# Optimization experiments

Measured on AMD Instinct MI355X. Metric: run time of the kernel, lower is better.

Reference implementation:

```python
import jax, jax.numpy as jnp
import numpy as np

N_NODES = 50000
N_EDGES = 1600000
IN_DIM = 128
HID = 128
SHARED = 64
N_GRAPHS = 2048


def setup_inputs() -> dict:
    key = jax.random.key(0)
    ks = jax.random.split(key, 16)
    x = jax.random.normal(ks[0], (N_NODES, IN_DIM), dtype=jnp.float32)
    edge_index = jax.random.randint(ks[1], (2, N_EDGES), 0, N_NODES, dtype=jnp.int64)
    batch = jnp.sort(jax.random.randint(ks[2], (N_NODES,), 0, N_GRAPHS, dtype=jnp.int64))

    def lin(k, fan_in, fan_out):
        bound = 1.0 / np.sqrt(fan_in)
        kw, kb = jax.random.split(k)
        W = jax.random.uniform(kw, (fan_in, fan_out), minval=-bound, maxval=bound, dtype=jnp.float32)
        b = jax.random.uniform(kb, (fan_out,), minval=-bound, maxval=bound, dtype=jnp.float32)
        return W, b

    W1a, b1a = lin(ks[3], IN_DIM, HID)
    W1b, b1b = lin(ks[4], HID, HID)
    W2a, b2a = lin(ks[5], HID, HID)
    W2b, b2b = lin(ks[6], HID, HID)
    Ws, bs = lin(ks[7], HID, SHARED)
    WlS, blS = lin(ks[8], SHARED, 1)
    WlP, blP = lin(ks[9], SHARED, 1)
    WnR, bnR = lin(ks[10], SHARED, 1)
    return dict(x=x, edge_index=edge_index, batch=batch,
                W1a=W1a, b1a=b1a, W1b=W1b, b1b=b1b,
                W2a=W2a, b2a=b2a, W2b=W2b, b2b=b2b,
                Ws=Ws, bs=bs, WlS=WlS, blS=blS, WlP=WlP, blP=blP, WnR=WnR, bnR=bnR)


def gin_conv(x, src, dst, Wa, ba, Wb, bb):
    # GINConv (eps=0): h_i = MLP(x_i + sum_{j->i} x_j)
    agg = jax.ops.segment_sum(x[src], dst, num_segments=N_NODES)
    h = x + agg
    h = jax.nn.relu(h @ Wa + ba)
    return h @ Wb + bb


def reference(x, edge_index, batch, W1a, b1a, W1b, b1b, W2a, b2a, W2b, b2b,
              Ws, bs, WlS, blS, WlP, blP, WnR, bnR):
    src, dst = edge_index[0], edge_index[1]
    h = jax.nn.relu(gin_conv(x, src, dst, W1a, b1a, W1b, b1b))
    h = jax.nn.relu(gin_conv(h, src, dst, W2a, b2a, W2b, b2b))
    # global mean pool over graph ids
    sums = jax.ops.segment_sum(h, batch, num_segments=N_GRAPHS)
    counts = jax.ops.segment_sum(jnp.ones((h.shape[0],), h.dtype), batch, num_segments=N_GRAPHS)
    pooled = sums / jnp.maximum(counts, 1.0)[:, None]
    g = jax.nn.relu(pooled @ Ws + bs)
    out_logS = (g @ WlS + blS)[:, 0]
    out_logP = (g @ WlP + blP)[:, 0]
    out_NR = (g @ WnR + bnR)[:, 0]
    return (out_logS, out_logP, out_NR)
```

## Files before the change

### kernel.cpp

```cpp
#include <hip/hip_runtime.h>
#include <hip/hip_bf16.h>


#define IN_DIM 128
#define NFINE 256
#define BIN_EPB 4096
#define SRCCH 16
#define NSLOT 3200
#define SPT 7

typedef float  f32x4  __attribute__((ext_vector_type(4)));
typedef short  bf16x4 __attribute__((ext_vector_type(4)));
typedef short  bf16x8 __attribute__((ext_vector_type(8)));

__device__ __forceinline__ unsigned short bf16_rne(float v) {
    unsigned u = __float_as_uint(v);
    unsigned t = u + 0x7fffu + ((u >> 16) & 1u);
    return (unsigned short)(t >> 16);
}


__global__ __launch_bounds__(256) void f32_to_bf16_kernel(
    const float4* __restrict__ in, uint4* __restrict__ out, int n8)
{
    int i = blockIdx.x * 256 + threadIdx.x;
    if (i >= n8) return;
    float4 a = in[i * 2];
    float4 b = in[i * 2 + 1];
    float v[8] = {a.x, a.y, a.z, a.w, b.x, b.y, b.z, b.w};
    unsigned r[4];
#pragma unroll
    for (int j = 0; j < 4; ++j)
        r[j] = (unsigned)bf16_rne(v[j * 2]) | ((unsigned)bf16_rne(v[j * 2 + 1]) << 16);
    out[i] = make_uint4(r[0], r[1], r[2], r[3]);
}


__global__ __launch_bounds__(256) void conv_weights_kernel(
    const float* __restrict__ W0, const float* __restrict__ W1,
    const float* __restrict__ W2, const float* __restrict__ W3,
    unsigned short* __restrict__ Wh, unsigned short* __restrict__ Wl)
{
    int m   = blockIdx.x >> 6;
    int idx = (blockIdx.x & 63) * 256 + threadIdx.x;
    const float* W = (m == 0) ? W0 : (m == 1) ? W1 : (m == 2) ? W2 : W3;
    int k = idx >> 7, n = idx & 127;
    float v = W[idx];
    unsigned short hh = bf16_rne(v);
    float hf = __uint_as_float(((unsigned)hh) << 16);
    unsigned short ll = bf16_rne(v - hf);
    Wh[m * 16384 + n * 128 + k] = hh;
    Wl[m * 16384 + n * 128 + k] = ll;
}


__device__ __forceinline__ int bucket_lo(int b, int n_nodes) {
    return (int)(((long long)b * n_nodes + NFINE - 1) / NFINE);
}

__global__ __launch_bounds__(256) void bin_kernel(
    const int* __restrict__ src, const int* __restrict__ dst,
    int* __restrict__ buckets, int* __restrict__ bcur,
    int n_edges, int n_nodes, int cap)
{
    __shared__ int cnt[NFINE];
    __shared__ int base[NFINE];
    cnt[threadIdx.x] = 0;
    __syncthreads();

    const int e0 = blockIdx.x * BIN_EPB + threadIdx.x * 16;
    int ne = n_edges - e0;
    if (ne < 0) ne = 0;
    if (ne > 16) ne = 16;

    int d[16], s[16], off[16];
    if (ne == 16) {
#pragma unroll
        for (int q = 0; q < 4; ++q) {
            int4 dv = *(const int4*)(dst + e0 + q * 4);
            int4 sv = *(const int4*)(src + e0 + q * 4);
            d[q * 4 + 0] = dv.x; d[q * 4 + 1] = dv.y;
            d[q * 4 + 2] = dv.z; d[q * 4 + 3] = dv.w;
            s[q * 4 + 0] = sv.x; s[q * 4 + 1] = sv.y;
            s[q * 4 + 2] = sv.z; s[q * 4 + 3] = sv.w;
        }
    } else {
#pragma unroll
        for (int j = 0; j < 16; ++j) {
            d[j] = (j < ne) ? dst[e0 + j] : 0;
            s[j] = (j < ne) ? src[e0 + j] : 0;
        }
    }
#pragma unroll
    for (int j = 0; j < 16; ++j)
        if (j < ne) {
            int b = (int)(((long long)d[j] * NFINE) / n_nodes);
            off[j] = atomicAdd(&cnt[b], 1);
        }
    __syncthreads();
    base[threadIdx.x] = atomicAdd(&bcur[threadIdx.x], cnt[threadIdx.x]);
    __syncthreads();
#pragma unroll
    for (int j = 0; j < 16; ++j)
        if (j < ne) {
            int b = (int)(((long long)d[j] * NFINE) / n_nodes);
            int pack = ((d[j] - bucket_lo(b, n_nodes)) << 16) | s[j];
            buckets[(size_t)b * cap + base[b] + off[j]] = pack;
        }
}

__global__ __launch_bounds__(512) void csr_fused_kernel(
    const int* __restrict__ buckets, const int* __restrict__ bcnt,
    int* __restrict__ row_start, int* __restrict__ csr_src,
    int cap, int n_nodes, int n_edges)
{
    __shared__ int bc[NFINE];
    __shared__ int h[NSLOT];
    __shared__ int tsum[512];
    __shared__ int bbase_s;

    const int b = blockIdx.x;
    const int t = threadIdx.x;
    const int lo_n = bucket_lo(b, n_nodes);
    const int hi_n = bucket_lo(b + 1, n_nodes);
    const int sl = hi_n - lo_n;

    if (t < NFINE) bc[t] = bcnt[t];
    for (int i = t; i < NSLOT; i += 512) h[i] = 0;
    __syncthreads();
    if (t == 0) {
        int s = 0;
        for (int i = 0; i < b; ++i) s += bc[i];
        bbase_s = s;
    }
    const int nb = bc[b];
    const int* bp = buckets + (size_t)b * cap;
    __syncthreads();

    for (int i = t; i < nb; i += 512) {
        int v = bp[i];
        int key = (v >> 16) * SRCCH + (int)(((long long)(v & 0xFFFF) * SRCCH) / n_nodes);
        atomicAdd(&h[key], 1);
    }
    __syncthreads();

    int base = 0;
#pragma unroll
    for (int j = 0; j < SPT; ++j) {
        int slot = t * SPT + j;
        if (slot < NSLOT) {
            int v = h[slot];
            h[slot] = base;
            base += v;
        }
    }
    tsum[t] = base;
    __syncthreads();
    for (int off = 1; off < 512; off <<= 1) {
        int tmp = (t >= off) ? tsum[t - off] : 0;
        __syncthreads();
        tsum[t] += tmp;
        __syncthreads();
    }
    int texcl = tsum[t] - base + bbase_s;
#pragma unroll
    for (int j = 0; j < SPT; ++j) {
        int slot = t * SPT + j;
        if (slot < NSLOT) h[slot] += texcl;
    }
    __syncthreads();
    for (int i = t; i < sl; i += 512) row_start[lo_n + i] = h[i * SRCCH];
    if (b == NFINE - 1 && t == 0) row_start[n_nodes] = n_edges;
    __syncthreads();

    for (int i = t; i < nb; i += 512) {
        int v = bp[i];
        int key = (v >> 16) * SRCCH + (int)(((long long)(v & 0xFFFF) * SRCCH) / n_nodes);
        csr_src[atomicAdd(&h[key], 1)] = v & 0xFFFF;
    }
}


__device__ __forceinline__ void add_row8(float acc[8], uint4 r) {
    union { unsigned u; float f; } c;
    c.u = r.x << 16;         acc[0] += c.f;
    c.u = r.x & 0xffff0000u; acc[1] += c.f;
    c.u = r.y << 16;         acc[2] += c.f;
    c.u = r.y & 0xffff0000u; acc[3] += c.f;
    c.u = r.z << 16;         acc[4] += c.f;
    c.u = r.z & 0xffff0000u; acc[5] += c.f;
    c.u = r.w << 16;         acc[6] += c.f;
    c.u = r.w & 0xffff0000u; acc[7] += c.f;
}

__global__ __launch_bounds__(256) void gather_agg_bf16_kernel(
    const float* __restrict__ xf,
    const uint4* __restrict__ xb,
    const int* __restrict__ row_start, const int* __restrict__ csr_src,
    float* __restrict__ out, int n_nodes)
{
    int t = blockIdx.x * 256 + threadIdx.x;
    int node = t >> 4;
    int lane = t & 15;
    if (node >= n_nodes) return;
    int lo = row_start[node];
    int hi = row_start[node + 1];

    const f32x4* xfr = (const f32x4*)(xf + (size_t)node * IN_DIM + lane * 8);
    f32x4 a0 = __builtin_nontemporal_load(xfr);
    f32x4 a1 = __builtin_nontemporal_load(xfr + 1);
    float acc[8] = {a0.x, a0.y, a0.z, a0.w, a1.x, a1.y, a1.z, a1.w};

    int e = lo;
    for (; e + 3 < hi; e += 4) {
        int s0 = csr_src[e];
        int s1 = csr_src[e + 1];
        int s2 = csr_src[e + 2];
        int s3 = csr_src[e + 3];
        uint4 r0 = xb[(size_t)s0 * 16 + lane];
        uint4 r1 = xb[(size_t)s1 * 16 + lane];
        uint4 r2 = xb[(size_t)s2 * 16 + lane];
        uint4 r3 = xb[(size_t)s3 * 16 + lane];
        add_row8(acc, r0);
        add_row8(acc, r1);
        add_row8(acc, r2);
        add_row8(acc, r3);
    }
    for (; e < hi; ++e) {
        uint4 r = xb[(size_t)csr_src[e] * 16 + lane];
        add_row8(acc, r);
    }

    f32x4 o0 = {acc[0], acc[1], acc[2], acc[3]};
    f32x4 o1 = {acc[4], acc[5], acc[6], acc[7]};
    f32x4* op = (f32x4*)(out + (size_t)node * IN_DIM + lane * 8);
    __builtin_nontemporal_store(o0, op);
    __builtin_nontemporal_store(o1, op + 1);
}

#define HSTRIDE 132

template <bool EMIT_BF16>
__global__ __launch_bounds__(256) void fused_mlp_kernel(
    const float* __restrict__ A,
    const unsigned short* __restrict__ Wa_h, const unsigned short* __restrict__ Wa_l,
    const float* __restrict__ ba,
    const unsigned short* __restrict__ Wb_h, const unsigned short* __restrict__ Wb_l,
    const float* __restrict__ bb,
    float* __restrict__ C, unsigned short* __restrict__ Cb, int M)
{
    __shared__ __align__(16) unsigned short Hh[64][HSTRIDE];
    __shared__ __align__(16) unsigned short Hl[64][HSTRIDE];

    const int t    = threadIdx.x;
    const int wave = t >> 6;
    const int lane = t & 63;
    const int l15  = lane & 15;
    const int quad = lane >> 4;
    const int rw   = (wave & 1) * 32;
    const int cw   = (wave >> 1) * 64;
    const int row0 = blockIdx.x * 64 + rw;

    bf16x8 ah[2][4], al[2][4];

#pragma unroll
    for (int ti = 0; ti < 2; ++ti) {
        int ar = row0 + ti * 16 + l15;
        const float* ap = A + (size_t)((ar < M) ? ar : (M - 1)) * IN_DIM + quad * 8;
        f32x4 av[8];
#pragma unroll
        for (int k0c = 0; k0c < 4; ++k0c) {
            av[k0c * 2]     = *(const f32x4*)(ap + k0c * 32);
            av[k0c * 2 + 1] = *(const f32x4*)(ap + k0c * 32 + 4);
        }
#pragma unroll
        for (int k0c = 0; k0c < 4; ++k0c) {
            float v[8] = {av[k0c * 2].x, av[k0c * 2].y, av[k0c * 2].z, av[k0c * 2].w,
                          av[k0c * 2 + 1].x, av[k0c * 2 + 1].y,
                          av[k0c * 2 + 1].z, av[k0c * 2 + 1].w};
            unsigned short hh[8], ll[8];
#pragma unroll
            for (int j = 0; j < 8; ++j) {
                unsigned short h = bf16_rne(v[j]);
                hh[j] = h;
                ll[j] = bf16_rne(v[j] - __uint_as_float(((unsigned)h) << 16));
            }
            ah[ti][k0c] = *(const bf16x8*)hh;
            al[ti][k0c] = *(const bf16x8*)ll;
        }
    }

    f32x4 acc[2][4];
#pragma unroll
    for (int ti = 0; ti < 2; ++ti)
#pragma unroll
        for (int ct = 0; ct < 4; ++ct) acc[ti][ct] = {0.f, 0.f, 0.f, 0.f};

#pragma unroll
    for (int ct = 0; ct < 4; ++ct) {
        const unsigned short* wph = Wa_h + (size_t)(cw + ct * 16 + l15) * IN_DIM + quad * 8;
        const unsigned short* wpl = Wa_l + (size_t)(cw + ct * 16 + l15) * IN_DIM + quad * 8;
        bf16x8 wh[4], wl[4];
#pragma unroll
        for (int k0c = 0; k0c < 4; ++k0c) {
            wh[k0c] = *(const bf16x8*)(wph + k0c * 32);
            wl[k0c] = *(const bf16x8*)(wpl + k0c * 32);
        }
#pragma unroll
        for (int k0c = 0; k0c < 4; ++k0c) {
            acc[0][ct] = __builtin_amdgcn_mfma_f32_16x16x32_bf16(ah[0][k0c], wh[k0c], acc[0][ct], 0, 0, 0);
            acc[1][ct] = __builtin_amdgcn_mfma_f32_16x16x32_bf16(ah[1][k0c], wh[k0c], acc[1][ct], 0, 0, 0);
            acc[0][ct] = __builtin_amdgcn_mfma_f32_16x16x32_bf16(al[0][k0c], wh[k0c], acc[0][ct], 0, 0, 0);
            acc[1][ct] = __builtin_amdgcn_mfma_f32_16x16x32_bf16(al[1][k0c], wh[k0c], acc[1][ct], 0, 0, 0);
            acc[0][ct] = __builtin_amdgcn_mfma_f32_16x16x32_bf16(ah[0][k0c], wl[k0c], acc[0][ct], 0, 0, 0);
            acc[1][ct] = __builtin_amdgcn_mfma_f32_16x16x32_bf16(ah[1][k0c], wl[k0c], acc[1][ct], 0, 0, 0);
        }
    }

#pragma unroll
    for (int ti = 0; ti < 2; ++ti) {
#pragma unroll
        for (int ct = 0; ct < 4; ++ct) {
            int col = cw + ct * 16 + l15;
            float b = ba[col];
#pragma unroll
            for (int r = 0; r < 4; ++r) {
                int rl = rw + ti * 16 + quad * 4 + r;
                float v = fmaxf(acc[ti][ct][r] + b, 0.f);
                unsigned short hh = bf16_rne(v);
                Hh[rl][col] = hh;
                Hl[rl][col] = bf16_rne(v - __uint_as_float(((unsigned)hh) << 16));
            }
            acc[ti][ct] = {0.f, 0.f, 0.f, 0.f};
        }
    }
    __syncthreads();

#pragma unroll
    for (int ti = 0; ti < 2; ++ti) {
        const int hr = rw + ti * 16 + l15;
#pragma unroll
        for (int k0c = 0; k0c < 4; ++k0c) {
            const int hk = k0c * 32 + quad * 8;
            bf16x4 h0 = *(const bf16x4*)&Hh[hr][hk];
            bf16x4 h1 = *(const bf16x4*)&Hh[hr][hk + 4];
            bf16x4 l0 = *(const bf16x4*)&Hl[hr][hk];
            bf16x4 l1 = *(const bf16x4*)&Hl[hr][hk + 4];
            ah[ti][k0c] = __builtin_shufflevector(h0, h1, 0, 1, 2, 3, 4, 5, 6, 7);
            al[ti][k0c] = __builtin_shufflevector(l0, l1, 0, 1, 2, 3, 4, 5, 6, 7);
        }
    }

#pragma unroll
    for (int ct = 0; ct < 4; ++ct) {
        const unsigned short* wph = Wb_h + (size_t)(cw + ct * 16 + l15) * IN_DIM + quad * 8;
        const unsigned short* wpl = Wb_l + (size_t)(cw + ct * 16 + l15) * IN_DIM + quad * 8;
        bf16x8 wh[4], wl[4];
#pragma unroll
        for (int k0c = 0; k0c < 4; ++k0c) {
            wh[k0c] = *(const bf16x8*)(wph + k0c * 32);
            wl[k0c] = *(const bf16x8*)(wpl + k0c * 32);
        }
#pragma unroll
        for (int k0c = 0; k0c < 4; ++k0c) {
            acc[0][ct] = __builtin_amdgcn_mfma_f32_16x16x32_bf16(ah[0][k0c], wh[k0c], acc[0][ct], 0, 0, 0);
            acc[1][ct] = __builtin_amdgcn_mfma_f32_16x16x32_bf16(ah[1][k0c], wh[k0c], acc[1][ct], 0, 0, 0);
            acc[0][ct] = __builtin_amdgcn_mfma_f32_16x16x32_bf16(al[0][k0c], wh[k0c], acc[0][ct], 0, 0, 0);
            acc[1][ct] = __builtin_amdgcn_mfma_f32_16x16x32_bf16(al[1][k0c], wh[k0c], acc[1][ct], 0, 0, 0);
            acc[0][ct] = __builtin_amdgcn_mfma_f32_16x16x32_bf16(ah[0][k0c], wl[k0c], acc[0][ct], 0, 0, 0);
            acc[1][ct] = __builtin_amdgcn_mfma_f32_16x16x32_bf16(ah[1][k0c], wl[k0c], acc[1][ct], 0, 0, 0);
        }
    }

#pragma unroll
    for (int ti = 0; ti < 2; ++ti) {
        const int rbase = row0 + ti * 16 + quad * 4;
#pragma unroll
        for (int ct = 0; ct < 4; ++ct) {
            int col = cw + ct * 16 + l15;
            float b = bb[col];
#pragma unroll
            for (int r = 0; r < 4; ++r) {
                int row = rbase + r;
                if (row < M) {
                    float o = fmaxf(acc[ti][ct][r] + b, 0.f);
                    C[(size_t)row * IN_DIM + col] = o;
                    if (EMIT_BF16)
                        Cb[(size_t)row * IN_DIM + col] = bf16_rne(o);
                }
            }
        }
    }
}


__device__ __forceinline__ int lower_bound_i(const int* __restrict__ a, int n, int v) {
    int lo = 0, hi = n;
    while (lo < hi) {
        int mid = (lo + hi) >> 1;
        if (a[mid] < v) lo = mid + 1; else hi = mid;
    }
    return lo;
}

__global__ __launch_bounds__(128) void pool_kernel(
    const float* __restrict__ h, const int* __restrict__ batch,
    float* __restrict__ pooled, int n_nodes, int n_graphs)
{
    int g = blockIdx.x;
    int lo = lower_bound_i(batch, n_nodes, g);
    int hi = lower_bound_i(batch, n_nodes, g + 1);
    int j = threadIdx.x;
    float acc = 0.f;
    for (int i = lo; i < hi; ++i)
        acc += h[(size_t)i * IN_DIM + j];
    float cnt = (float)(hi - lo);
    pooled[(size_t)g * IN_DIM + j] = acc / fmaxf(cnt, 1.0f);
}

__global__ __launch_bounds__(64) void head_kernel(
    const float* __restrict__ pooled,
    const float* __restrict__ Ws,  const float* __restrict__ bs,
    const float* __restrict__ WlS, const float* __restrict__ blS,
    const float* __restrict__ WlP, const float* __restrict__ blP,
    const float* __restrict__ WnR, const float* __restrict__ bnR,
    float* __restrict__ out, int n_graphs)
{
    int g = blockIdx.x;
    int j = threadIdx.x;
    const float* p = pooled + (size_t)g * IN_DIM;
    float acc = bs[j];
#pragma unroll 8
    for (int k = 0; k < IN_DIM; ++k)
        acc = fmaf(p[k], Ws[k * 64 + j], acc);
    float gj = fmaxf(acc, 0.f);
    float s1 = gj * WlS[j];
    float s2 = gj * WlP[j];
    float s3 = gj * WnR[j];
#pragma unroll
    for (int off = 32; off > 0; off >>= 1) {
        s1 += __shfl_down(s1, off);
        s2 += __shfl_down(s2, off);
        s3 += __shfl_down(s3, off);
    }
    if (j == 0) {
        out[g]                = s1 + blS[0];
        out[n_graphs + g]     = s2 + blP[0];
        out[2 * n_graphs + g] = s3 + bnR[0];
    }
}


extern "C" void kernel_launch(void* const* d_in, const int* in_sizes, int n_in,
                              void* d_out, int out_size, void* d_ws, size_t ws_size,
                              hipStream_t stream)
{
    const float* x   = (const float*)d_in[0];
    const int*   ei  = (const int*)d_in[1];
    const int*   bat = (const int*)d_in[2];
    const float* W1a = (const float*)d_in[3];
    const float* b1a = (const float*)d_in[4];
    const float* W1b = (const float*)d_in[5];
    const float* b1b = (const float*)d_in[6];
    const float* W2a = (const float*)d_in[7];
    const float* b2a = (const float*)d_in[8];
    const float* W2b = (const float*)d_in[9];
    const float* b2b = (const float*)d_in[10];
    const float* Ws  = (const float*)d_in[11];
    const float* bs  = (const float*)d_in[12];
    const float* WlS = (const float*)d_in[13];
    const float* blS = (const float*)d_in[14];
    const float* WlP = (const float*)d_in[15];
    const float* blP = (const float*)d_in[16];
    const float* WnR = (const float*)d_in[17];
    const float* bnR = (const float*)d_in[18];

    const int n_nodes  = in_sizes[0] / IN_DIM;
    const int n_edges  = in_sizes[1] / 2;
    const int n_graphs = out_size / 3;
    const int* src = ei;
    const int* dst = ei + n_edges;

    const size_t node_elems   = (size_t)n_nodes * IN_DIM;
    const size_t pooled_elems = (size_t)n_graphs * IN_DIM;

    float* xbf    = (float*)d_ws;
    float* buf2   = xbf  + node_elems;
    float* bufA   = buf2 + node_elems;
    float* pooled = bufA + node_elems;
    int* row_start = (int*)(pooled + pooled_elems);
    int* bcur      = row_start + (n_nodes + 1);
    int* csr_src   = bcur + NFINE;
    unsigned short* wt_h = (unsigned short*)(csr_src + n_edges);
    unsigned short* wt_l = wt_h + 4 * 16384;

    unsigned short* xb = (unsigned short*)xbf;
    const int cap = n_edges / NFINE + 1024;
    int* buckets = (int*)bufA;

    const int gatherblocks = (int)(((size_t)n_nodes * 16 + 255) / 256);
    const int mlpblocks = (n_nodes + 63) / 64;
    const int binblocks = (n_edges + BIN_EPB - 1) / BIN_EPB;
    const int n8 = (int)(node_elems / 8);
    const int cvtblocks = (n8 + 255) / 256;

    conv_weights_kernel<<<256, 256, 0, stream>>>(W1a, W1b, W2a, W2b, wt_h, wt_l);
    hipMemsetAsync(bcur, 0, NFINE * sizeof(int), stream);
    bin_kernel<<<binblocks, 256, 0, stream>>>(src, dst, buckets, bcur,
                                              n_edges, n_nodes, cap);
    csr_fused_kernel<<<NFINE, 512, 0, stream>>>(buckets, bcur, row_start,
                                                csr_src, cap, n_nodes, n_edges);

    f32_to_bf16_kernel<<<cvtblocks, 256, 0, stream>>>((const float4*)x, (uint4*)xb, n8);
    gather_agg_bf16_kernel<<<gatherblocks, 256, 0, stream>>>(
        x, (const uint4*)xb, row_start, csr_src, bufA, n_nodes);
    fused_mlp_kernel<true><<<mlpblocks, 256, 0, stream>>>(
        bufA, wt_h, wt_l, b1a, wt_h + 16384, wt_l + 16384, b1b,
        buf2, xb, n_nodes);

    gather_agg_bf16_kernel<<<gatherblocks, 256, 0, stream>>>(
        buf2, (const uint4*)xb, row_start, csr_src, bufA, n_nodes);
    fused_mlp_kernel<false><<<mlpblocks, 256, 0, stream>>>(
        bufA, wt_h + 2 * 16384, wt_l + 2 * 16384, b2a,
        wt_h + 3 * 16384, wt_l + 3 * 16384, b2b,
        buf2, nullptr, n_nodes);

    pool_kernel<<<n_graphs, 128, 0, stream>>>(buf2, bat, pooled, n_nodes, n_graphs);
    head_kernel<<<n_graphs, 64, 0, stream>>>(pooled, Ws, bs, WlS, blS, WlP, blP,
                                             WnR, bnR, (float*)d_out, n_graphs);
}
```

Measured before the change: 375.8 us.

## Fuse neighbor gather-aggregation into GIN MLP kernel via shared-memory staging

Merges the separate gather-aggregate kernel into the fused MLP kernel. Each 64-row block first sums its rows' self features and bf16 neighbor rows, then writes the hi/lo bf16 split into LDS, where the MFMA stages read it. This removes the fp32 aggregate round-trip through global memory and two launches per layer. The second layer reads from a separate bf16 copy so it can overwrite buf2 in place. The cost is fewer independent gather threads in flight per CU, because LDS use grows and each block walks its 64 nodes in four serial passes, so the random-access gather may hide latency less well.

Result: slower. 419.6 us (+11.6%).

```diff
diff --git a/kernel.cpp b/kernel.cpp
--- a/kernel.cpp
+++ b/kernel.cpp
@@ -8,9 +8,9 @@
 #define SRCCH 16
 #define NSLOT 3200
 #define SPT 7
+#define HSTRIDE 136
 
 typedef float  f32x4  __attribute__((ext_vector_type(4)));
-typedef short  bf16x4 __attribute__((ext_vector_type(4)));
 typedef short  bf16x8 __attribute__((ext_vector_type(8)));
 
 __device__ __forceinline__ unsigned short bf16_rne(float v) {
@@ -193,66 +193,67 @@
     c.u = r.w & 0xffff0000u; acc[7] += c.f;
 }
 
-__global__ __launch_bounds__(256) void gather_agg_bf16_kernel(
-    const float* __restrict__ xf,
+template <bool EMIT_BF16>
+__global__ __launch_bounds__(256) void fused_gin_layer_kernel(
+    const float* __restrict__ Aself,
     const uint4* __restrict__ xb,
     const int* __restrict__ row_start, const int* __restrict__ csr_src,
-    float* __restrict__ out, int n_nodes)
-{
-    int t = blockIdx.x * 256 + threadIdx.x;
-    int node = t >> 4;
-    int lane = t & 15;
-    if (node >= n_nodes) return;
-    int lo = row_start[node];
-    int hi = row_start[node + 1];
-
-    const f32x4* xfr = (const f32x4*)(xf + (size_t)node * IN_DIM + lane * 8);
-    f32x4 a0 = __builtin_nontemporal_load(xfr);
-    f32x4 a1 = __builtin_nontemporal_load(xfr + 1);
-    float acc[8] = {a0.x, a0.y, a0.z, a0.w, a1.x, a1.y, a1.z, a1.w};
-
-    int e = lo;
-    for (; e + 3 < hi; e += 4) {
-        int s0 = csr_src[e];
-        int s1 = csr_src[e + 1];
-        int s2 = csr_src[e + 2];
-        int s3 = csr_src[e + 3];
-        uint4 r0 = xb[(size_t)s0 * 16 + lane];
-        uint4 r1 = xb[(size_t)s1 * 16 + lane];
-        uint4 r2 = xb[(size_t)s2 * 16 + lane];
-        uint4 r3 = xb[(size_t)s3 * 16 + lane];
-        add_row8(acc, r0);
-        add_row8(acc, r1);
-        add_row8(acc, r2);
-        add_row8(acc, r3);
-    }
-    for (; e < hi; ++e) {
-        uint4 r = xb[(size_t)csr_src[e] * 16 + lane];
-        add_row8(acc, r);
-    }
-
-    f32x4 o0 = {acc[0], acc[1], acc[2], acc[3]};
-    f32x4 o1 = {acc[4], acc[5], acc[6], acc[7]};
-    f32x4* op = (f32x4*)(out + (size_t)node * IN_DIM + lane * 8);
-    __builtin_nontemporal_store(o0, op);
-    __builtin_nontemporal_store(o1, op + 1);
-}
-
-#define HSTRIDE 132
-
-template <bool EMIT_BF16>
-__global__ __launch_bounds__(256) void fused_mlp_kernel(
-    const float* __restrict__ A,
     const unsigned short* __restrict__ Wa_h, const unsigned short* __restrict__ Wa_l,
     const float* __restrict__ ba,
     const unsigned short* __restrict__ Wb_h, const unsigned short* __restrict__ Wb_l,
     const float* __restrict__ bb,
     float* __restrict__ C, unsigned short* __restrict__ Cb, int M)
 {
-    __shared__ __align__(16) unsigned short Hh[64][HSTRIDE];
-    __shared__ __align__(16) unsigned short Hl[64][HSTRIDE];
-
-    const int t    = threadIdx.x;
+    __shared__ __align__(16) unsigned short Ah[64][HSTRIDE];
+    __shared__ __align__(16) unsigned short Al[64][HSTRIDE];
+
+    const int t = threadIdx.x;
+
+    {
+        const int gl = t & 15;
+        const int gn = t >> 4;
+        for (int rl = gn; rl < 64; rl += 16) {
+            const int node = blockIdx.x * 64 + rl;
+            float acc[8] = {0.f, 0.f, 0.f, 0.f, 0.f, 0.f, 0.f, 0.f};
+            if (node < M) {
+                const f32x4* sp = (const f32x4*)(Aself + (size_t)node * IN_DIM + gl * 8);
+                f32x4 a0 = sp[0];
+                f32x4 a1 = sp[1];
+                acc[0] = a0.x; acc[1] = a0.y; acc[2] = a0.z; acc[3] = a0.w;
+                acc[4] = a1.x; acc[5] = a1.y; acc[6] = a1.z; acc[7] = a1.w;
+                int lo = row_start[node];
+                int hi = row_start[node + 1];
+                int e = lo;
+                for (; e + 3 < hi; e += 4) {
+                    int s0 = csr_src[e];
+                    int s1 = csr_src[e + 1];
+                    int s2 = csr_src[e + 2];
+                    int s3 = csr_src[e + 3];
+                    uint4 r0 = xb[(size_t)s0 * 16 + gl];
+                    uint4 r1 = xb[(size_t)s1 * 16 + gl];
+                    uint4 r2 = xb[(size_t)s2 * 16 + gl];
+                    uint4 r3 = xb[(size_t)s3 * 16 + gl];
+                    add_row8(acc, r0);
+                    add_row8(acc, r1);
+                    add_row8(acc, r2);
+                    add_row8(acc, r3);
+                }
+                for (; e < hi; ++e)
+                    add_row8(acc, xb[(size_t)csr_src[e] * 16 + gl]);
+            }
+            unsigned short hh[8], ll[8];
+#pragma unroll
+            for (int j = 0; j < 8; ++j) {
+                unsigned short h = bf16_rne(acc[j]);
+                hh[j] = h;
+                ll[j] = bf16_rne(acc[j] - __uint_as_float(((unsigned)h) << 16));
+            }
+            *(uint4*)&Ah[rl][gl * 8] = *(uint4*)hh;
+            *(uint4*)&Al[rl][gl * 8] = *(uint4*)ll;
+        }
+    }
+    __syncthreads();
+
     const int wave = t >> 6;
     const int lane = t & 63;
     const int l15  = lane & 15;
@@ -262,33 +263,17 @@
     const int row0 = blockIdx.x * 64 + rw;
 
     bf16x8 ah[2][4], al[2][4];
-
 #pragma unroll
     for (int ti = 0; ti < 2; ++ti) {
-        int ar = row0 + ti * 16 + l15;
-        const float* ap = A + (size_t)((ar < M) ? ar : (M - 1)) * IN_DIM + quad * 8;
-        f32x4 av[8];
+        const int hr = rw + ti * 16 + l15;
 #pragma unroll
         for (int k0c = 0; k0c < 4; ++k0c) {
-            av[k0c * 2]     = *(const f32x4*)(ap + k0c * 32);
-            av[k0c * 2 + 1] = *(const f32x4*)(ap + k0c * 32 + 4);
-        }
-#pragma unroll
-        for (int k0c = 0; k0c < 4; ++k0c) {
-            float v[8] = {av[k0c * 2].x, av[k0c * 2].y, av[k0c * 2].z, av[k0c * 2].w,
-                          av[k0c * 2 + 1].x, av[k0c * 2 + 1].y,
-                          av[k0c * 2 + 1].z, av[k0c * 2 + 1].w};
-            unsigned short hh[8], ll[8];
-#pragma unroll
-            for (int j = 0; j < 8; ++j) {
-                unsigned short h = bf16_rne(v[j]);
-                hh[j] = h;
-                ll[j] = bf16_rne(v[j] - __uint_as_float(((unsigned)h) << 16));
-            }
-            ah[ti][k0c] = *(const bf16x8*)hh;
-            al[ti][k0c] = *(const bf16x8*)ll;
-        }
-    }
+            const int hk = k0c * 32 + quad * 8;
+            ah[ti][k0c] = *(const bf16x8*)&Ah[hr][hk];
+            al[ti][k0c] = *(const bf16x8*)&Al[hr][hk];
+        }
+    }
+    __syncthreads();
 
     f32x4 acc[2][4];
 #pragma unroll
@@ -328,8 +313,8 @@
                 int rl = rw + ti * 16 + quad * 4 + r;
                 float v = fmaxf(acc[ti][ct][r] + b, 0.f);
                 unsigned short hh = bf16_rne(v);
-                Hh[rl][col] = hh;
-                Hl[rl][col] = bf16_rne(v - __uint_as_float(((unsigned)hh) << 16));
+                Ah[rl][col] = hh;
+                Al[rl][col] = bf16_rne(v - __uint_as_float(((unsigned)hh) << 16));
             }
             acc[ti][ct] = {0.f, 0.f, 0.f, 0.f};
         }
@@ -342,12 +327,8 @@
 #pragma unroll
         for (int k0c = 0; k0c < 4; ++k0c) {
             const int hk = k0c * 32 + quad * 8;
-            bf16x4 h0 = *(const bf16x4*)&Hh[hr][hk];
-            bf16x4 h1 = *(const bf16x4*)&Hh[hr][hk + 4];
-            bf16x4 l0 = *(const bf16x4*)&Hl[hr][hk];
-            bf16x4 l1 = *(const bf16x4*)&Hl[hr][hk + 4];
-            ah[ti][k0c] = __builtin_shufflevector(h0, h1, 0, 1, 2, 3, 4, 5, 6, 7);
-            al[ti][k0c] = __builtin_shufflevector(l0, l1, 0, 1, 2, 3, 4, 5, 6, 7);
+            ah[ti][k0c] = *(const bf16x8*)&Ah[hr][hk];
+            al[ti][k0c] = *(const bf16x8*)&Al[hr][hk];
         }
     }
 
@@ -494,12 +475,12 @@
     unsigned short* wt_h = (unsigned short*)(csr_src + n_edges);
     unsigned short* wt_l = wt_h + 4 * 16384;
 
-    unsigned short* xb = (unsigned short*)xbf;
+    unsigned short* xb  = (unsigned short*)xbf;
+    unsigned short* xb2 = xb + node_elems;
     const int cap = n_edges / NFINE + 1024;
     int* buckets = (int*)bufA;
 
-    const int gatherblocks = (int)(((size_t)n_nodes * 16 + 255) / 256);
-    const int mlpblocks = (n_nodes + 63) / 64;
+    const int layerblocks = (n_nodes + 63) / 64;
     const int binblocks = (n_edges + BIN_EPB - 1) / BIN_EPB;
     const int n8 = (int)(node_elems / 8);
     const int cvtblocks = (n8 + 255) / 256;
@@ -512,16 +493,14 @@
                                                 csr_src, cap, n_nodes, n_edges);
 
     f32_to_bf16_kernel<<<cvtblocks, 256, 0, stream>>>((const float4*)x, (uint4*)xb, n8);
-    gather_agg_bf16_kernel<<<gatherblocks, 256, 0, stream>>>(
-        x, (const uint4*)xb, row_start, csr_src, bufA, n_nodes);
-    fused_mlp_kernel<true><<<mlpblocks, 256, 0, stream>>>(
-        bufA, wt_h, wt_l, b1a, wt_h + 16384, wt_l + 16384, b1b,
-        buf2, xb, n_nodes);
-
-    gather_agg_bf16_kernel<<<gatherblocks, 256, 0, stream>>>(
-        buf2, (const uint4*)xb, row_start, csr_src, bufA, n_nodes);
-    fused_mlp_kernel<false><<<mlpblocks, 256, 0, stream>>>(
-        bufA, wt_h + 2 * 16384, wt_l + 2 * 16384, b2a,
+    fused_gin_layer_kernel<true><<<layerblocks, 256, 0, stream>>>(
+        x, (const uint4*)xb, row_start, csr_src,
+        wt_h, wt_l, b1a, wt_h + 16384, wt_l + 16384, b1b,
+        buf2, xb2, n_nodes);
+
+    fused_gin_layer_kernel<false><<<layerblocks, 256, 0, stream>>>(
+        buf2, (const uint4*)xb2, row_start, csr_src,
+        wt_h + 2 * 16384, wt_l + 2 * 16384, b2a,
         wt_h + 3 * 16384, wt_l + 3 * 16384, b2b,
         buf2, nullptr, n_nodes);
 
```
